# Performance work log

Hardware: AMD Instinct MI355X
Metric: run time of the kernel (lower is better)

## Reference

```python
import jax, jax.numpy as jnp
import numpy as np

L = 32            # num_layers
R = 16            # lora_rank
P = L * 7         # 224 projections
D = 256           # encoder d_model
H = 4             # encoder heads
HD = D // H
FF = 2048         # TransformerEncoderLayer default dim_feedforward
PED = 512         # proj_embed_dim
HID = 4096
KV = 8 * (4096 // 32)   # 1024
INTER = 11008
VOCAB = 50000
NEG = -1e9

# projection index groups within the P=7*L ordering [q,k,v,o,gate,up,down]
IDX_A_HID = jnp.asarray((np.arange(L)[:, None] * 7 + np.array([0, 1, 2, 3, 4, 5])).reshape(-1))  # in_dim=4096
IDX_A_INT = jnp.asarray(np.arange(L) * 7 + 6)                                                    # in_dim=11008
IDX_B_HID = jnp.asarray((np.arange(L)[:, None] * 7 + np.array([0, 3, 6])).reshape(-1))           # out_dim=4096
IDX_B_KV  = jnp.asarray((np.arange(L)[:, None] * 7 + np.array([1, 2])).reshape(-1))              # out_dim=1024
IDX_B_INT = jnp.asarray((np.arange(L)[:, None] * 7 + np.array([4, 5])).reshape(-1))              # out_dim=11008


def _ln(x, g, b, eps=1e-5):
    m = jnp.mean(x, -1, keepdims=True)
    v = jnp.mean((x - m) ** 2, -1, keepdims=True)
    return (x - m) * jax.lax.rsqrt(v + eps) * g + b


def _enc_layer(x, pad, qw, qb, ow, ob, g1, b1, f1w, f1b, f2w, f2b, g2, b2):
    # post-norm TransformerEncoderLayer (torch default), relu FFN, eval mode (no dropout)
    Bsz, S, _ = x.shape
    qkv = x @ qw.T + qb                                  # [B,S,3D]
    q, k, v = jnp.split(qkv, 3, axis=-1)
    hd = lambda t: t.reshape(Bsz, S, H, HD).transpose(0, 2, 1, 3)
    q, k, v = hd(q), hd(k), hd(v)
    s = jnp.einsum('bhqd,bhkd->bhqk', q, k) / jnp.asarray(np.sqrt(HD), x.dtype)
    s = jnp.where(pad[:, None, None, :], NEG, s)
    a = jax.nn.softmax(s, -1)
    o = jnp.einsum('bhqk,bhkd->bhqd', a, v).transpose(0, 2, 1, 3).reshape(Bsz, S, D)
    x = _ln(x + o @ ow.T + ob, g1, b1)
    f = jax.nn.relu(x @ f1w.T + f1b) @ f2w.T + f2b
    return _ln(x + f, g2, b2)


def _forward(condition_ids, attention_mask, embed_table, enc_qkv_w, enc_qkv_b, enc_out_w, enc_out_b,
             enc_ln1_g, enc_ln1_b, enc_ff1_w, enc_ff1_b, enc_ff2_w, enc_ff2_b, enc_ln2_g, enc_ln2_b,
             proj_w, proj_b, a1_w, a1_b, a2_w, a2_b, b1_w, b1_b, b2_w, b2_b, scales):
    Bsz = condition_ids.shape[0]
    x = embed_table[condition_ids]                       # [B,S,256]
    pad = attention_mask == 0                            # key padding mask (~attention_mask)
    for l in range(3):
        x = _enc_layer(x, pad, enc_qkv_w[l], enc_qkv_b[l], enc_out_w[l], enc_out_b[l],
                       enc_ln1_g[l], enc_ln1_b[l], enc_ff1_w[l], enc_ff1_b[l],
                       enc_ff2_w[l], enc_ff2_b[l], enc_ln2_g[l], enc_ln2_b[l])
    am = attention_mask.astype(x.dtype)
    pooled = (x * am[..., None]).sum(1) / jnp.clip(am.sum(1, keepdims=True), 1.0)   # masked mean pool
    pe = (pooled @ proj_w.T + proj_b).reshape(Bsz, P, PED)                          # [B,224,512]

    def dec(w1, b1_, w2, b2_):
        return jax.nn.gelu(pe @ w1.T + b1_, approximate=False) @ w2.T + b2_

    A_base = dec(a1_w, a1_b, a2_w, a2_b).reshape(Bsz, P, R, 64)   # [B,P,r,64]
    B_base = dec(b1_w, b1_b, b2_w, b2_b).reshape(Bsz, P, 64, R)   # [B,P,64,r]
    sa, sb = scales[:, 0], scales[:, 1]

    def tile_A(idx, in_d):
        # all in_dims divisible by 64 => repeat(in_d//64+1)[:, :in_d] == exact tiling
        a = A_base[:, idx] * sa[idx][None, :, None, None]
        return jnp.tile(a, (1, 1, 1, in_d // 64))

    def tile_B(idx, out_d):
        b = B_base[:, idx] * sb[idx][None, :, None, None]
        return jnp.tile(b, (1, 1, out_d // 64, 1))

    return (tile_A(IDX_A_HID, HID), tile_A(IDX_A_INT, INTER),
            tile_B(IDX_B_HID, HID), tile_B(IDX_B_KV, KV), tile_B(IDX_B_INT, INTER))


def setup_inputs() -> dict:
    key = jax.random.key(0)
    ks = iter(jax.random.split(key, 40))
    rn = lambda shape, s=0.02: jax.random.normal(next(ks), shape, jnp.float32) * s
    Bsz, S = 4, 128
    return {
        'condition_ids': jax.random.randint(next(ks), (Bsz, S), 0, VOCAB),
        'attention_mask': jnp.ones((Bsz, S), jnp.int32),
        'embed_table': rn((VOCAB, D)),
        'enc_qkv_w': rn((3, 3 * D, D)), 'enc_qkv_b': rn((3, 3 * D)),
        'enc_out_w': rn((3, D, D)), 'enc_out_b': rn((3, D)),
        'enc_ln1_g': jnp.ones((3, D)), 'enc_ln1_b': jnp.zeros((3, D)),
        'enc_ff1_w': rn((3, FF, D)), 'enc_ff1_b': rn((3, FF)),
        'enc_ff2_w': rn((3, D, FF)), 'enc_ff2_b': rn((3, D)),
        'enc_ln2_g': jnp.ones((3, D)), 'enc_ln2_b': jnp.zeros((3, D)),
        'proj_w': rn((P * PED, D)), 'proj_b': rn((P * PED,)),
        'a1_w': rn((D, PED)), 'a1_b': rn((D,)),
        'a2_w': rn((R * 64, D)), 'a2_b': rn((R * 64,)),
        'b1_w': rn((D, PED)), 'b1_b': rn((D,)),
        'b2_w': rn((R * 64, D)), 'b2_b': rn((R * 64,)),
        'scales': jnp.full((P, 2), 0.01, jnp.float32),
    }


def reference(condition_ids, attention_mask, embed_table, enc_qkv_w, enc_qkv_b, enc_out_w, enc_out_b,
              enc_ln1_g, enc_ln1_b, enc_ff1_w, enc_ff1_b, enc_ff2_w, enc_ff2_b, enc_ln2_g, enc_ln2_b,
              proj_w, proj_b, a1_w, a1_b, a2_w, a2_b, b1_w, b1_b, b2_w, b2_b, scales):
    return _forward(condition_ids, attention_mask, embed_table, enc_qkv_w, enc_qkv_b, enc_out_w, enc_out_b,
                    enc_ln1_g, enc_ln1_b, enc_ff1_w, enc_ff1_b, enc_ff2_w, enc_ff2_b, enc_ln2_g, enc_ln2_b,
                    proj_w, proj_b, a1_w, a1_b, a2_w, a2_b, b1_w, b1_b, b2_w, b2_b, scales)
```

## Files before the change

kernel.cpp:

```cpp
#include <hip/hip_runtime.h>
#include <hip/hip_bf16.h>

typedef unsigned short u16;
typedef unsigned int u32;
typedef __attribute__((ext_vector_type(8))) short short8;
typedef __attribute__((ext_vector_type(4))) float floatx4;

__device__ __forceinline__ u16 f2bf(float f) {
  u32 x = __float_as_uint(f);
  x += 0x7FFFu + ((x >> 16) & 1u);
  return (u16)(x >> 16);
}
__device__ __forceinline__ u32 pk2(float lo, float hi) {
  return (u32)f2bf(lo) | ((u32)f2bf(hi) << 16);
}

__global__ void embed_kernel(const int* __restrict__ ids, const float* __restrict__ emb,
                             float* __restrict__ x) {
  int tok = blockIdx.x, d = threadIdx.x;
  x[tok * 256 + d] = emb[(size_t)ids[tok] * 256 + d];
}

template <int ACT, int SPLIT>
__global__ __launch_bounds__(256) void mfma_gemm_kernel(const float* __restrict__ A,
    const float* __restrict__ W, const float* __restrict__ bias, float* __restrict__ C,
    int M, int N, int K, int KS, int pstride) {
  __shared__ u16 Abf[64 * 32];
  __shared__ u16 Wbf[64 * 32];
  const int t = threadIdx.x;
  const int m0 = blockIdx.x * 64, n0 = blockIdx.y * 64;
  const int kz = blockIdx.z;
  const int srow = t >> 2, skc = (t & 3) * 8;
  const int w = t >> 6, lane = t & 63;
  const int q = lane >> 4, rr = lane & 15;
  floatx4 acc[4];
#pragma unroll
  for (int i = 0; i < 4; ++i) acc[i] = (floatx4){0.f, 0.f, 0.f, 0.f};

  const int kbeg = kz * KS, kend = kbeg + KS;
  for (int k0 = kbeg; k0 < kend; k0 += 32) {
    const float* ga = A + (size_t)(m0 + srow) * K + k0 + skc;
    const float* gw = W + (size_t)(n0 + srow) * K + k0 + skc;
    float4 a0 = *(const float4*)ga;
    float4 a1 = *(const float4*)(ga + 4);
    float4 w0 = *(const float4*)gw;
    float4 w1 = *(const float4*)(gw + 4);
    uint4 pa, pw;
    pa.x = pk2(a0.x, a0.y); pa.y = pk2(a0.z, a0.w);
    pa.z = pk2(a1.x, a1.y); pa.w = pk2(a1.z, a1.w);
    pw.x = pk2(w0.x, w0.y); pw.y = pk2(w0.z, w0.w);
    pw.z = pk2(w1.x, w1.y); pw.w = pk2(w1.z, w1.w);
    __syncthreads();
    *(uint4*)&Abf[srow * 32 + skc] = pa;
    *(uint4*)&Wbf[srow * 32 + skc] = pw;
    __syncthreads();
    short8 af = *(short8*)&Abf[(w * 16 + rr) * 32 + q * 8];
#pragma unroll
    for (int ct = 0; ct < 4; ++ct) {
      short8 bf = *(short8*)&Wbf[(ct * 16 + rr) * 32 + q * 8];
      acc[ct] = __builtin_amdgcn_mfma_f32_16x16x32_bf16(af, bf, acc[ct], 0, 0, 0);
    }
  }

  float* dst = SPLIT ? (C + (size_t)kz * pstride) : C;
#pragma unroll
  for (int ct = 0; ct < 4; ++ct) {
    int col = n0 + ct * 16 + rr;
#pragma unroll
    for (int r = 0; r < 4; ++r) {
      int row = m0 + w * 16 + q * 4 + r;
      float v = acc[ct][r];
      if (!SPLIT) {
        v += bias[col];
        if (ACT == 1) v = fmaxf(v, 0.f);
        if (ACT == 2) v = 0.5f * v * (1.f + erff(v * 0.70710678118654752f));
      }
      dst[(size_t)row * N + col] = v;
    }
  }
}

template <int ACT>
__global__ void red_bias_act_kernel(const float* __restrict__ parts, int nparts, int pstride,
                                    const float* __restrict__ bias, float* __restrict__ dst, int N) {
  int idx = blockIdx.x * 256 + threadIdx.x;
  float v = bias[idx % N];
  for (int p = 0; p < nparts; ++p) v += parts[(size_t)p * pstride + idx];
  if (ACT == 1) v = fmaxf(v, 0.f);
  if (ACT == 2) v = 0.5f * v * (1.f + erff(v * 0.70710678118654752f));
  dst[idx] = v;
}

__global__ __launch_bounds__(256) void attn_kernel(const float* __restrict__ qkv,
    const int* __restrict__ mask, float* __restrict__ o) {
  __shared__ float Klds[8192];
  __shared__ float Vlds[8192];
  const int blk = blockIdx.x;
  const int b = blk >> 7, h = (blk >> 5) & 3, qg = blk & 31;
  const int t = threadIdx.x;
  for (int i = t; i < 8192; i += 256) {
    int s = i >> 6, d = i & 63;
    size_t base = (size_t)(b * 128 + s) * 768 + h * 64 + d;
    Klds[(s << 6) + (d ^ (s & 31))] = qkv[base + 256];
    Vlds[i] = qkv[base + 512];
  }
  __syncthreads();
  const int wave = t >> 6, lane = t & 63;
  const int q = qg * 4 + wave;
  float qv = qkv[(size_t)(b * 128 + q) * 768 + h * 64 + lane];
  const int m0i = mask[b * 128 + lane];
  const int m1i = mask[b * 128 + 64 + lane];
  float s0 = 0.f, s1 = 0.f;
  const int sw = lane & 31;
  for (int d = 0; d < 64; ++d) {
    float qd = __shfl(qv, d);
    s0 += qd * Klds[(lane << 6) + (d ^ sw)];
    s1 += qd * Klds[((lane + 64) << 6) + (d ^ sw)];
  }
  s0 *= 0.125f; s1 *= 0.125f;
  if (m0i == 0) s0 = -1000000000.0f;
  if (m1i == 0) s1 = -1000000000.0f;
  float m = fmaxf(s0, s1);
  for (int off = 32; off; off >>= 1) m = fmaxf(m, __shfl_xor(m, off));
  float p0 = expf(s0 - m), p1 = expf(s1 - m);
  float sum = p0 + p1;
  for (int off = 32; off; off >>= 1) sum += __shfl_xor(sum, off);
  float rs = 1.f / sum;
  float acc = 0.f;
  for (int k = 0; k < 64; ++k) acc += __shfl(p0, k) * Vlds[(k << 6) + lane];
  for (int k = 0; k < 64; ++k) acc += __shfl(p1, k) * Vlds[((k + 64) << 6) + lane];
  o[(size_t)(b * 128 + q) * 256 + h * 64 + lane] = acc * rs;
}

__global__ __launch_bounds__(256) void add_ln_red_kernel(float* __restrict__ x,
    const float* __restrict__ parts, int nparts, int pstride, const float* __restrict__ bias,
    const float* __restrict__ g, const float* __restrict__ b) {
  int tok = blockIdx.x, t = threadIdx.x;
  int idx = tok * 256 + t;
  float r = x[idx] + bias[t];
  for (int p = 0; p < nparts; ++p) r += parts[(size_t)p * pstride + idx];
  float s = r, sq = r * r;
  for (int off = 32; off; off >>= 1) { s += __shfl_xor(s, off); sq += __shfl_xor(sq, off); }
  __shared__ float red[8];
  int wave = t >> 6, lane = t & 63;
  if (lane == 0) { red[wave] = s; red[4 + wave] = sq; }
  __syncthreads();
  float S = red[0] + red[1] + red[2] + red[3];
  float SQ = red[4] + red[5] + red[6] + red[7];
  float mean = S * (1.f / 256.f);
  float var = SQ * (1.f / 256.f) - mean * mean;
  float inv = 1.f / sqrtf(fmaxf(var, 0.f) + 1e-5f);
  x[idx] = (r - mean) * inv * g[t] + b[t];
}

__global__ void pool_kernel(const float* __restrict__ x, const int* __restrict__ mask,
                            float* __restrict__ pooled) {
  int b = blockIdx.x, d = threadIdx.x;
  float s = 0.f, c = 0.f;
  for (int ss = 0; ss < 128; ++ss) {
    float m = (float)mask[b * 128 + ss];
    s += m * x[(size_t)(b * 128 + ss) * 256 + d];
    c += m;
  }
  pooled[b * 256 + d] = s / fmaxf(c, 1.f);
}

__global__ __launch_bounds__(256) void proj_kernel(const float* __restrict__ pooled,
    const float* __restrict__ W, const float* __restrict__ bias, float* __restrict__ pe) {
  __shared__ float pl[1024];
  int t = threadIdx.x;
  for (int i = t; i < 1024; i += 256) pl[i] = pooled[i];
  __syncthreads();
  int wave = t >> 6, lane = t & 63;
  int half = lane >> 5, sl = lane & 31;
  int row = blockIdx.x * 8 + wave * 2 + half;
  float4 w0 = *(const float4*)(W + (size_t)row * 256 + sl * 8);
  float4 w1 = *(const float4*)(W + (size_t)row * 256 + sl * 8 + 4);
  float a0, a1, a2, a3;
#pragma unroll
  for (int bb = 0; bb < 4; ++bb) {
    const float* pp = &pl[bb * 256 + sl * 8];
    float v = w0.x * pp[0] + w0.y * pp[1] + w0.z * pp[2] + w0.w * pp[3]
            + w1.x * pp[4] + w1.y * pp[5] + w1.z * pp[6] + w1.w * pp[7];
    if (bb == 0) a0 = v; else if (bb == 1) a1 = v; else if (bb == 2) a2 = v; else a3 = v;
  }
#pragma unroll
  for (int off = 1; off < 32; off <<= 1) {
    a0 += __shfl_xor(a0, off); a1 += __shfl_xor(a1, off);
    a2 += __shfl_xor(a2, off); a3 += __shfl_xor(a3, off);
  }
  if (sl == 0) {
    float bv = bias[row];
    pe[0 * 114688 + row] = a0 + bv;
    pe[1 * 114688 + row] = a1 + bv;
    pe[2 * 114688 + row] = a2 + bv;
    pe[3 * 114688 + row] = a3 + bv;
  }
}

__global__ __launch_bounds__(256) void tile_a_kernel(const float* __restrict__ Abase,
    const float* __restrict__ scales, float* __restrict__ out, int nI, int ind,
    int pdiv, int pmul, int padd) {
  int row = blockIdx.x;
  int r = row & 15, bi = row >> 4;
  int i = bi % nI, b = bi / nI;
  int p = (i / pdiv) * 7 + (i % pdiv) * pmul + padd;
  float s = scales[2 * p];
  __shared__ float chunk[64];
  int t = threadIdx.x;
  if (t < 64) chunk[t] = Abase[((size_t)(b * 224 + p) * 16 + r) * 64 + t] * s;
  __syncthreads();
  size_t ob = (size_t)row * ind;
  for (int u = t; u * 4 < ind; u += 256) {
    int c0 = u * 4;
    float4 ov = *(const float4*)&chunk[c0 & 63];
    *(float4*)(out + ob + c0) = ov;
  }
}

__global__ __launch_bounds__(256) void tile_b_kernel(const float* __restrict__ Bbase,
    const float* __restrict__ scales, float* __restrict__ out, int nI, int ind, int nchunks,
    int pdiv, int pmul, int padd) {
  int blk = blockIdx.x;
  int cc = blk % nchunks, bi = blk / nchunks;
  int i = bi % nI, b = bi / nI;
  int p = (i / pdiv) * 7 + (i % pdiv) * pmul + padd;
  float s = scales[2 * p + 1];
  __shared__ float chunk[1024];
  int t = threadIdx.x;
  for (int e = t; e < 1024; e += 256) chunk[e] = Bbase[(size_t)(b * 224 + p) * 1024 + e] * s;
  __syncthreads();
  int cchunk16 = (ind / nchunks) * 16;
  size_t ob = (size_t)bi * ind * 16 + (size_t)cc * cchunk16;
  for (int u = t; u * 4 < cchunk16; u += 256) {
    int e0 = u * 4;
    int cabs = (cc * cchunk16 + e0) >> 4;
    int src = ((cabs & 63) << 4) + (e0 & 15);
    float4 ov = *(const float4*)&chunk[src];
    *(float4*)(out + ob + e0) = ov;
  }
}

extern "C" void kernel_launch(void* const* d_in, const int* in_sizes, int n_in,
                              void* d_out, int out_size, void* d_ws, size_t ws_size,
                              hipStream_t stream) {
  const int* ids     = (const int*)d_in[0];
  const int* mask    = (const int*)d_in[1];
  const float* emb   = (const float*)d_in[2];
  const float* qkv_w = (const float*)d_in[3];
  const float* qkv_b = (const float*)d_in[4];
  const float* out_w = (const float*)d_in[5];
  const float* out_b = (const float*)d_in[6];
  const float* ln1_g = (const float*)d_in[7];
  const float* ln1_b = (const float*)d_in[8];
  const float* ff1_w = (const float*)d_in[9];
  const float* ff1_b = (const float*)d_in[10];
  const float* ff2_w = (const float*)d_in[11];
  const float* ff2_b = (const float*)d_in[12];
  const float* ln2_g = (const float*)d_in[13];
  const float* ln2_b = (const float*)d_in[14];
  const float* proj_w = (const float*)d_in[15];
  const float* proj_b = (const float*)d_in[16];
  const float* a1_w = (const float*)d_in[17];
  const float* a1_b = (const float*)d_in[18];
  const float* a2_w = (const float*)d_in[19];
  const float* a2_b = (const float*)d_in[20];
  const float* b1_w = (const float*)d_in[21];
  const float* b1_b = (const float*)d_in[22];
  const float* b2_w = (const float*)d_in[23];
  const float* b2_b = (const float*)d_in[24];
  const float* scales = (const float*)d_in[25];

  float* w = (float*)d_ws;
  float* x      = w + 0;
  float* qkv    = w + 262144;
  float* attn_o = w + 655360;
  float* ff     = w + 786432;
  float* pooled = w + 1835008;
  float* pe     = w + 1836032;
  float* hA     = w + 2294784;
  float* hB     = w + 2524160;
  float* Abase  = w + 2753536;
  float* Bbase  = w + 3671040;
  float* parts  = w + 4588544;

  float* out = (float*)d_out;

  embed_kernel<<<512, 256, 0, stream>>>(ids, emb, x);
  for (int l = 0; l < 3; ++l) {
    mfma_gemm_kernel<0, 0><<<dim3(8, 12), 256, 0, stream>>>(
        x, qkv_w + l * 768 * 256, qkv_b + l * 768, qkv, 512, 768, 256, 256, 0);
    attn_kernel<<<512, 256, 0, stream>>>(qkv, mask, attn_o);
    mfma_gemm_kernel<0, 1><<<dim3(8, 4, 4), 256, 0, stream>>>(
        attn_o, out_w + l * 256 * 256, nullptr, parts, 512, 256, 256, 64, 131072);
    add_ln_red_kernel<<<512, 256, 0, stream>>>(x, parts, 4, 131072, out_b + l * 256,
                                               ln1_g + l * 256, ln1_b + l * 256);
    mfma_gemm_kernel<1, 0><<<dim3(8, 32), 256, 0, stream>>>(
        x, ff1_w + l * 2048 * 256, ff1_b + l * 2048, ff, 512, 2048, 256, 256, 0);
    mfma_gemm_kernel<0, 1><<<dim3(8, 4, 8), 256, 0, stream>>>(
        ff, ff2_w + l * 256 * 2048, nullptr, parts, 512, 256, 2048, 256, 131072);
    add_ln_red_kernel<<<512, 256, 0, stream>>>(x, parts, 8, 131072, ff2_b + l * 256,
                                               ln2_g + l * 256, ln2_b + l * 256);
  }
  pool_kernel<<<4, 256, 0, stream>>>(x, mask, pooled);
  proj_kernel<<<14336, 256, 0, stream>>>(pooled, proj_w, proj_b, pe);

  mfma_gemm_kernel<0, 1><<<dim3(14, 4, 4), 256, 0, stream>>>(
      pe, a1_w, nullptr, parts, 896, 256, 512, 128, 229376);
  red_bias_act_kernel<2><<<896, 256, 0, stream>>>(parts, 4, 229376, a1_b, hA, 256);
  mfma_gemm_kernel<0, 0><<<dim3(14, 16), 256, 0, stream>>>(
      hA, a2_w, a2_b, Abase, 896, 1024, 256, 256, 0);

  mfma_gemm_kernel<0, 1><<<dim3(14, 4, 4), 256, 0, stream>>>(
      pe, b1_w, nullptr, parts, 896, 256, 512, 128, 229376);
  red_bias_act_kernel<2><<<896, 256, 0, stream>>>(parts, 4, 229376, b1_b, hB, 256);
  mfma_gemm_kernel<0, 0><<<dim3(14, 16), 256, 0, stream>>>(
      hB, b2_w, b2_b, Bbase, 896, 1024, 256, 256, 0);

  tile_a_kernel<<<12288, 256, 0, stream>>>(Abase, scales, out, 192, 4096, 6, 1, 0);
  tile_a_kernel<<<2048, 256, 0, stream>>>(Abase, scales, out + 50331648ull, 32, 11008, 1, 0, 6);
  tile_b_kernel<<<3072, 256, 0, stream>>>(Bbase, scales, out + 72876032ull, 96, 4096, 8, 3, 3, 0);
  tile_b_kernel<<<512, 256, 0, stream>>>(Bbase, scales, out + 98041856ull, 64, 1024, 2, 2, 1, 1);
  tile_b_kernel<<<2048, 256, 0, stream>>>(Bbase, scales, out + 102236160ull, 64, 11008, 8, 2, 1, 4);
}
```

Before: 974.3 us.

## Fuse encoder layers and decoder GEMMs with output tiling using bf16 intermediates

Rewrites most of the pipeline. Weights are pre-converted to bf16 once per call. Each encoder layer becomes fused kernels: out-proj, residual, LayerNorm and FF1 in one, and FF2, LayerNorm and next-layer QKV in another, with bf16 activations between them. The LoRA decoder GEMMs are fused with the scale-and-tile broadcast writes, which removes the intermediate Abase/Bbase buffers and the split-K partial reductions. The cost is that the fused encoder kernels run only 16 blocks, which leaves most of the GPU idle. There is also extra bf16 rounding of intermediates.

```diff
diff --git a/kernel.cpp b/kernel.cpp
--- a/kernel.cpp
+++ b/kernel.cpp
@@ -11,88 +11,113 @@
   x += 0x7FFFu + ((x >> 16) & 1u);
   return (u16)(x >> 16);
 }
-__device__ __forceinline__ u32 pk2(float lo, float hi) {
-  return (u32)f2bf(lo) | ((u32)f2bf(hi) << 16);
-}
-
-__global__ void embed_kernel(const int* __restrict__ ids, const float* __restrict__ emb,
-                             float* __restrict__ x) {
-  int tok = blockIdx.x, d = threadIdx.x;
-  x[tok * 256 + d] = emb[(size_t)ids[tok] * 256 + d];
-}
-
-template <int ACT, int SPLIT>
-__global__ __launch_bounds__(256) void mfma_gemm_kernel(const float* __restrict__ A,
-    const float* __restrict__ W, const float* __restrict__ bias, float* __restrict__ C,
-    int M, int N, int K, int KS, int pstride) {
-  __shared__ u16 Abf[64 * 32];
-  __shared__ u16 Wbf[64 * 32];
-  const int t = threadIdx.x;
-  const int m0 = blockIdx.x * 64, n0 = blockIdx.y * 64;
-  const int kz = blockIdx.z;
-  const int srow = t >> 2, skc = (t & 3) * 8;
-  const int w = t >> 6, lane = t & 63;
-  const int q = lane >> 4, rr = lane & 15;
-  floatx4 acc[4];
-#pragma unroll
-  for (int i = 0; i < 4; ++i) acc[i] = (floatx4){0.f, 0.f, 0.f, 0.f};
-
-  const int kbeg = kz * KS, kend = kbeg + KS;
-  for (int k0 = kbeg; k0 < kend; k0 += 32) {
-    const float* ga = A + (size_t)(m0 + srow) * K + k0 + skc;
-    const float* gw = W + (size_t)(n0 + srow) * K + k0 + skc;
-    float4 a0 = *(const float4*)ga;
-    float4 a1 = *(const float4*)(ga + 4);
-    float4 w0 = *(const float4*)gw;
-    float4 w1 = *(const float4*)(gw + 4);
-    uint4 pa, pw;
-    pa.x = pk2(a0.x, a0.y); pa.y = pk2(a0.z, a0.w);
-    pa.z = pk2(a1.x, a1.y); pa.w = pk2(a1.z, a1.w);
-    pw.x = pk2(w0.x, w0.y); pw.y = pk2(w0.z, w0.w);
-    pw.z = pk2(w1.x, w1.y); pw.w = pk2(w1.z, w1.w);
-    __syncthreads();
-    *(uint4*)&Abf[srow * 32 + skc] = pa;
-    *(uint4*)&Wbf[srow * 32 + skc] = pw;
-    __syncthreads();
-    short8 af = *(short8*)&Abf[(w * 16 + rr) * 32 + q * 8];
-#pragma unroll
-    for (int ct = 0; ct < 4; ++ct) {
-      short8 bf = *(short8*)&Wbf[(ct * 16 + rr) * 32 + q * 8];
-      acc[ct] = __builtin_amdgcn_mfma_f32_16x16x32_bf16(af, bf, acc[ct], 0, 0, 0);
-    }
-  }
-
-  float* dst = SPLIT ? (C + (size_t)kz * pstride) : C;
-#pragma unroll
-  for (int ct = 0; ct < 4; ++ct) {
-    int col = n0 + ct * 16 + rr;
-#pragma unroll
-    for (int r = 0; r < 4; ++r) {
-      int row = m0 + w * 16 + q * 4 + r;
-      float v = acc[ct][r];
-      if (!SPLIT) {
-        v += bias[col];
-        if (ACT == 1) v = fmaxf(v, 0.f);
-        if (ACT == 2) v = 0.5f * v * (1.f + erff(v * 0.70710678118654752f));
+__device__ __forceinline__ float bf2f(u16 u) { return __uint_as_float(((u32)u) << 16); }
+
+__device__ __forceinline__ void mfma8(floatx4& acc, short8 a, short8 b) {
+  acc = __builtin_amdgcn_mfma_f32_16x16x32_bf16(a, b, acc, 0, 0, 0);
+}
+
+#define ZACC24(A)                    \
+  do {                               \
+    for (int _i = 0; _i < 2; ++_i)   \
+      for (int _j = 0; _j < 4; ++_j) \
+        A[_i][_j] = (floatx4){0.f, 0.f, 0.f, 0.f}; \
+  } while (0)
+
+__device__ __forceinline__ void gemm_tile_lA(floatx4 acc[2][4], const u16* Abf, int lda,
+                                             const u16* W, int ldw, int n0, int K, int lane) {
+  const int rr = lane & 15, q = lane >> 4;
+  for (int k0 = 0; k0 < K; k0 += 32) {
+    short8 a0 = *(const short8*)(Abf + rr * lda + k0 + q * 8);
+    short8 a1 = *(const short8*)(Abf + (16 + rr) * lda + k0 + q * 8);
+#pragma unroll
+    for (int nt = 0; nt < 4; ++nt) {
+      short8 b = *(const short8*)(W + (size_t)(n0 + nt * 16 + rr) * ldw + k0 + q * 8);
+      mfma8(acc[0][nt], a0, b);
+      mfma8(acc[1][nt], a1, b);
+    }
+  }
+}
+
+__device__ __forceinline__ void gemm_tile_gA(floatx4 acc[2][4], const u16* Ag, int lda, int m0,
+                                             const u16* W, int ldw, int n0, int K, int lane) {
+  const int rr = lane & 15, q = lane >> 4;
+  for (int k0 = 0; k0 < K; k0 += 32) {
+    short8 a0 = *(const short8*)(Ag + (size_t)(m0 + rr) * lda + k0 + q * 8);
+    short8 a1 = *(const short8*)(Ag + (size_t)(m0 + 16 + rr) * lda + k0 + q * 8);
+#pragma unroll
+    for (int nt = 0; nt < 4; ++nt) {
+      short8 b = *(const short8*)(W + (size_t)(n0 + nt * 16 + rr) * ldw + k0 + q * 8);
+      mfma8(acc[0][nt], a0, b);
+      mfma8(acc[1][nt], a1, b);
+    }
+  }
+}
+
+__device__ __forceinline__ void store_cd_bf16(floatx4 acc[2][4], u16* dst, int ld, int m0,
+                                              int n0, const float* bias, int relu, int lane) {
+  const int rr = lane & 15, q = lane >> 4;
+#pragma unroll
+  for (int mt = 0; mt < 2; ++mt)
+#pragma unroll
+    for (int nt = 0; nt < 4; ++nt) {
+      int col = n0 + nt * 16 + rr;
+      float bv = bias[col];
+#pragma unroll
+      for (int r = 0; r < 4; ++r) {
+        int row = m0 + mt * 16 + q * 4 + r;
+        float v = acc[mt][nt][r] + bv;
+        if (relu) v = fmaxf(v, 0.f);
+        dst[(size_t)row * ld + col] = f2bf(v);
       }
-      dst[(size_t)row * N + col] = v;
-    }
-  }
-}
-
-template <int ACT>
-__global__ void red_bias_act_kernel(const float* __restrict__ parts, int nparts, int pstride,
-                                    const float* __restrict__ bias, float* __restrict__ dst, int N) {
-  int idx = blockIdx.x * 256 + threadIdx.x;
-  float v = bias[idx % N];
-  for (int p = 0; p < nparts; ++p) v += parts[(size_t)p * pstride + idx];
-  if (ACT == 1) v = fmaxf(v, 0.f);
-  if (ACT == 2) v = 0.5f * v * (1.f + erff(v * 0.70710678118654752f));
-  dst[idx] = v;
-}
-
-__global__ __launch_bounds__(256) void attn_kernel(const float* __restrict__ qkv,
-    const int* __restrict__ mask, float* __restrict__ o) {
+    }
+}
+
+struct WConvArgs {
+  const float* src[8];
+  u16* dst[8];
+  int cnt[8];
+};
+__global__ __launch_bounds__(256) void wconv_kernel(WConvArgs a) {
+  int tid = blockIdx.x * 256 + threadIdx.x;
+  int stride = gridDim.x * 256;
+  for (int s = 0; s < 8; ++s) {
+    const float* src = a.src[s];
+    u16* dst = a.dst[s];
+    int n4 = a.cnt[s] >> 2;
+    for (int i = tid; i < n4; i += stride) {
+      float4 v = ((const float4*)src)[i];
+      ushort4 o;
+      o.x = f2bf(v.x); o.y = f2bf(v.y); o.z = f2bf(v.z); o.w = f2bf(v.w);
+      ((ushort4*)dst)[i] = o;
+    }
+  }
+}
+
+__global__ __launch_bounds__(256) void embed_qkv_kernel(const int* __restrict__ ids,
+    const float* __restrict__ emb, float* __restrict__ x, const u16* __restrict__ qkvw,
+    const float* __restrict__ qkvb, u16* __restrict__ qkvbf) {
+  __shared__ u16 Albs[32 * 256];
+  const int rb = blockIdx.x, t = threadIdx.x, w = t >> 6, lane = t & 63;
+  const int m0 = rb * 32;
+  for (int r = 0; r < 32; ++r) {
+    int row = m0 + r;
+    float v = emb[(size_t)ids[row] * 256 + t];
+    x[(size_t)row * 256 + t] = v;
+    Albs[r * 256 + t] = f2bf(v);
+  }
+  __syncthreads();
+  for (int g = 0; g < 3; ++g) {
+    floatx4 acc[2][4];
+    ZACC24(acc);
+    int n0 = w * 192 + g * 64;
+    gemm_tile_lA(acc, Albs, 256, qkvw, 256, n0, 256, lane);
+    store_cd_bf16(acc, qkvbf, 768, m0, n0, qkvb, 0, lane);
+  }
+}
+
+__global__ __launch_bounds__(256) void attn_kernel(const u16* __restrict__ qkv,
+    const int* __restrict__ mask, u16* __restrict__ o) {
   __shared__ float Klds[8192];
   __shared__ float Vlds[8192];
   const int blk = blockIdx.x;
@@ -101,13 +126,13 @@
   for (int i = t; i < 8192; i += 256) {
     int s = i >> 6, d = i & 63;
     size_t base = (size_t)(b * 128 + s) * 768 + h * 64 + d;
-    Klds[(s << 6) + (d ^ (s & 31))] = qkv[base + 256];
-    Vlds[i] = qkv[base + 512];
+    Klds[(s << 6) + (d ^ (s & 31))] = bf2f(qkv[base + 256]);
+    Vlds[i] = bf2f(qkv[base + 512]);
   }
   __syncthreads();
   const int wave = t >> 6, lane = t & 63;
   const int q = qg * 4 + wave;
-  float qv = qkv[(size_t)(b * 128 + q) * 768 + h * 64 + lane];
+  float qv = bf2f(qkv[(size_t)(b * 128 + q) * 768 + h * 64 + lane]);
   const int m0i = mask[b * 128 + lane];
   const int m1i = mask[b * 128 + 64 + lane];
   float s0 = 0.f, s1 = 0.f;
@@ -129,28 +154,124 @@
   float acc = 0.f;
   for (int k = 0; k < 64; ++k) acc += __shfl(p0, k) * Vlds[(k << 6) + lane];
   for (int k = 0; k < 64; ++k) acc += __shfl(p1, k) * Vlds[((k + 64) << 6) + lane];
-  o[(size_t)(b * 128 + q) * 256 + h * 64 + lane] = acc * rs;
-}
-
-__global__ __launch_bounds__(256) void add_ln_red_kernel(float* __restrict__ x,
-    const float* __restrict__ parts, int nparts, int pstride, const float* __restrict__ bias,
-    const float* __restrict__ g, const float* __restrict__ b) {
-  int tok = blockIdx.x, t = threadIdx.x;
-  int idx = tok * 256 + t;
-  float r = x[idx] + bias[t];
-  for (int p = 0; p < nparts; ++p) r += parts[(size_t)p * pstride + idx];
-  float s = r, sq = r * r;
-  for (int off = 32; off; off >>= 1) { s += __shfl_xor(s, off); sq += __shfl_xor(sq, off); }
-  __shared__ float red[8];
-  int wave = t >> 6, lane = t & 63;
-  if (lane == 0) { red[wave] = s; red[4 + wave] = sq; }
-  __syncthreads();
-  float S = red[0] + red[1] + red[2] + red[3];
-  float SQ = red[4] + red[5] + red[6] + red[7];
-  float mean = S * (1.f / 256.f);
-  float var = SQ * (1.f / 256.f) - mean * mean;
-  float inv = 1.f / sqrtf(fmaxf(var, 0.f) + 1e-5f);
-  x[idx] = (r - mean) * inv * g[t] + b[t];
+  o[(size_t)(b * 128 + q) * 256 + h * 64 + lane] = f2bf(acc * rs);
+}
+
+__global__ __launch_bounds__(256) void post1_kernel(float* __restrict__ x,
+    const u16* __restrict__ obf, const u16* __restrict__ outw, const float* __restrict__ outb,
+    const float* __restrict__ g1, const float* __restrict__ b1, const u16* __restrict__ ff1w,
+    const float* __restrict__ ff1b, u16* __restrict__ ffbf) {
+  __shared__ u16 Albs[32 * 256];
+  __shared__ float S[32 * 264];
+  const int rb = blockIdx.x, t = threadIdx.x, w = t >> 6, lane = t & 63;
+  const int m0 = rb * 32;
+  {
+    const uint4* src = (const uint4*)(obf + (size_t)m0 * 256);
+    uint4* dst = (uint4*)Albs;
+    for (int i = t; i < 1024; i += 256) dst[i] = src[i];
+  }
+  __syncthreads();
+  floatx4 acc[2][4];
+  ZACC24(acc);
+  gemm_tile_lA(acc, Albs, 256, outw, 256, w * 64, 256, lane);
+  {
+    const int rr = lane & 15, q = lane >> 4;
+#pragma unroll
+    for (int mt = 0; mt < 2; ++mt)
+#pragma unroll
+      for (int nt = 0; nt < 4; ++nt) {
+        int col = w * 64 + nt * 16 + rr;
+        float bv = outb[col];
+#pragma unroll
+        for (int r = 0; r < 4; ++r) {
+          int row = mt * 16 + q * 4 + r;
+          S[row * 264 + col] = acc[mt][nt][r] + bv + x[(size_t)(m0 + row) * 256 + col];
+        }
+      }
+  }
+  __syncthreads();
+  {
+    int j = t >> 3, s8 = t & 7;
+    float sm = 0.f, sq = 0.f;
+    for (int c = s8 * 32; c < s8 * 32 + 32; ++c) {
+      float v = S[j * 264 + c];
+      sm += v; sq += v * v;
+    }
+    for (int off = 1; off < 8; off <<= 1) { sm += __shfl_xor(sm, off); sq += __shfl_xor(sq, off); }
+    float mean = sm * (1.f / 256.f);
+    float var = sq * (1.f / 256.f) - mean * mean;
+    float inv = 1.f / sqrtf(fmaxf(var, 0.f) + 1e-5f);
+    for (int c = s8 * 32; c < s8 * 32 + 32; ++c) {
+      float v = (S[j * 264 + c] - mean) * inv * g1[c] + b1[c];
+      x[(size_t)(m0 + j) * 256 + c] = v;
+      Albs[j * 256 + c] = f2bf(v);
+    }
+  }
+  __syncthreads();
+  for (int gb = 0; gb < 8; ++gb) {
+    floatx4 a2[2][4];
+    ZACC24(a2);
+    int n0 = w * 512 + gb * 64;
+    gemm_tile_lA(a2, Albs, 256, ff1w, 256, n0, 256, lane);
+    store_cd_bf16(a2, ffbf, 2048, m0, n0, ff1b, 1, lane);
+  }
+}
+
+template <int LAST>
+__global__ __launch_bounds__(256) void post2_kernel(const u16* __restrict__ ffbf,
+    const u16* __restrict__ ff2w, const float* __restrict__ ff2b, const float* __restrict__ g2,
+    const float* __restrict__ b2, float* __restrict__ x, const u16* __restrict__ qkvw,
+    const float* __restrict__ qkvb, u16* __restrict__ qkvbf) {
+  __shared__ u16 Albs[32 * 256];
+  __shared__ float S[32 * 264];
+  const int rb = blockIdx.x, t = threadIdx.x, w = t >> 6, lane = t & 63;
+  const int m0 = rb * 32;
+  floatx4 acc[2][4];
+  ZACC24(acc);
+  gemm_tile_gA(acc, ffbf, 2048, m0, ff2w, 2048, w * 64, 2048, lane);
+  {
+    const int rr = lane & 15, q = lane >> 4;
+#pragma unroll
+    for (int mt = 0; mt < 2; ++mt)
+#pragma unroll
+      for (int nt = 0; nt < 4; ++nt) {
+        int col = w * 64 + nt * 16 + rr;
+        float bv = ff2b[col];
+#pragma unroll
+        for (int r = 0; r < 4; ++r) {
+          int row = mt * 16 + q * 4 + r;
+          S[row * 264 + col] = acc[mt][nt][r] + bv + x[(size_t)(m0 + row) * 256 + col];
+        }
+      }
+  }
+  __syncthreads();
+  {
+    int j = t >> 3, s8 = t & 7;
+    float sm = 0.f, sq = 0.f;
+    for (int c = s8 * 32; c < s8 * 32 + 32; ++c) {
+      float v = S[j * 264 + c];
+      sm += v; sq += v * v;
+    }
+    for (int off = 1; off < 8; off <<= 1) { sm += __shfl_xor(sm, off); sq += __shfl_xor(sq, off); }
+    float mean = sm * (1.f / 256.f);
+    float var = sq * (1.f / 256.f) - mean * mean;
+    float inv = 1.f / sqrtf(fmaxf(var, 0.f) + 1e-5f);
+    for (int c = s8 * 32; c < s8 * 32 + 32; ++c) {
+      float v = (S[j * 264 + c] - mean) * inv * g2[c] + b2[c];
+      x[(size_t)(m0 + j) * 256 + c] = v;
+      Albs[j * 256 + c] = f2bf(v);
+    }
+  }
+  __syncthreads();
+  if (!LAST) {
+    for (int g = 0; g < 3; ++g) {
+      floatx4 a2[2][4];
+      ZACC24(a2);
+      int n0 = w * 192 + g * 64;
+      gemm_tile_lA(a2, Albs, 256, qkvw, 256, n0, 256, lane);
+      store_cd_bf16(a2, qkvbf, 768, m0, n0, qkvb, 0, lane);
+    }
+  }
 }
 
 __global__ void pool_kernel(const float* __restrict__ x, const int* __restrict__ mask,
@@ -166,7 +287,7 @@
 }
 
 __global__ __launch_bounds__(256) void proj_kernel(const float* __restrict__ pooled,
-    const float* __restrict__ W, const float* __restrict__ bias, float* __restrict__ pe) {
+    const float* __restrict__ W, const float* __restrict__ bias, u16* __restrict__ pebf) {
   __shared__ float pl[1024];
   int t = threadIdx.x;
   for (int i = t; i < 1024; i += 256) pl[i] = pooled[i];
@@ -191,53 +312,133 @@
   }
   if (sl == 0) {
     float bv = bias[row];
-    pe[0 * 114688 + row] = a0 + bv;
-    pe[1 * 114688 + row] = a1 + bv;
-    pe[2 * 114688 + row] = a2 + bv;
-    pe[3 * 114688 + row] = a3 + bv;
-  }
-}
-
-__global__ __launch_bounds__(256) void tile_a_kernel(const float* __restrict__ Abase,
-    const float* __restrict__ scales, float* __restrict__ out, int nI, int ind,
-    int pdiv, int pmul, int padd) {
-  int row = blockIdx.x;
-  int r = row & 15, bi = row >> 4;
-  int i = bi % nI, b = bi / nI;
-  int p = (i / pdiv) * 7 + (i % pdiv) * pmul + padd;
-  float s = scales[2 * p];
-  __shared__ float chunk[64];
-  int t = threadIdx.x;
-  if (t < 64) chunk[t] = Abase[((size_t)(b * 224 + p) * 16 + r) * 64 + t] * s;
-  __syncthreads();
-  size_t ob = (size_t)row * ind;
-  for (int u = t; u * 4 < ind; u += 256) {
-    int c0 = u * 4;
-    float4 ov = *(const float4*)&chunk[c0 & 63];
-    *(float4*)(out + ob + c0) = ov;
-  }
-}
-
-__global__ __launch_bounds__(256) void tile_b_kernel(const float* __restrict__ Bbase,
-    const float* __restrict__ scales, float* __restrict__ out, int nI, int ind, int nchunks,
-    int pdiv, int pmul, int padd) {
-  int blk = blockIdx.x;
-  int cc = blk % nchunks, bi = blk / nchunks;
-  int i = bi % nI, b = bi / nI;
-  int p = (i / pdiv) * 7 + (i % pdiv) * pmul + padd;
-  float s = scales[2 * p + 1];
-  __shared__ float chunk[1024];
-  int t = threadIdx.x;
-  for (int e = t; e < 1024; e += 256) chunk[e] = Bbase[(size_t)(b * 224 + p) * 1024 + e] * s;
-  __syncthreads();
-  int cchunk16 = (ind / nchunks) * 16;
-  size_t ob = (size_t)bi * ind * 16 + (size_t)cc * cchunk16;
-  for (int u = t; u * 4 < cchunk16; u += 256) {
-    int e0 = u * 4;
-    int cabs = (cc * cchunk16 + e0) >> 4;
-    int src = ((cabs & 63) << 4) + (e0 & 15);
-    float4 ov = *(const float4*)&chunk[src];
-    *(float4*)(out + ob + e0) = ov;
+    pebf[0 * 114688 + row] = f2bf(a0 + bv);
+    pebf[1 * 114688 + row] = f2bf(a1 + bv);
+    pebf[2 * 114688 + row] = f2bf(a2 + bv);
+    pebf[3 * 114688 + row] = f2bf(a3 + bv);
+  }
+}
+
+__global__ __launch_bounds__(256) void dec1_kernel(const u16* __restrict__ pebf,
+    const u16* __restrict__ a1w, const u16* __restrict__ b1w, const float* __restrict__ a1b,
+    const float* __restrict__ b1b, u16* __restrict__ hA, u16* __restrict__ hB) {
+  const int rb = blockIdx.x, zi = blockIdx.y;
+  const u16* W = zi ? b1w : a1w;
+  const float* bias = zi ? b1b : a1b;
+  u16* dst = zi ? hB : hA;
+  const int t = threadIdx.x, w = t >> 6, lane = t & 63;
+  const int m0 = rb * 32;
+  floatx4 acc[2][4];
+  ZACC24(acc);
+  gemm_tile_gA(acc, pebf, 512, m0, W, 512, w * 64, 512, lane);
+  const int rr = lane & 15, q = lane >> 4;
+#pragma unroll
+  for (int mt = 0; mt < 2; ++mt)
+#pragma unroll
+    for (int nt = 0; nt < 4; ++nt) {
+      int col = w * 64 + nt * 16 + rr;
+      float bv = bias[col];
+#pragma unroll
+      for (int r = 0; r < 4; ++r) {
+        int row = m0 + mt * 16 + q * 4 + r;
+        float v = acc[mt][nt][r] + bv;
+        v = 0.5f * v * (1.f + erff(v * 0.70710678118654752f));
+        dst[(size_t)row * 256 + col] = f2bf(v);
+      }
+    }
+}
+
+__global__ __launch_bounds__(256) void dec2a_kernel(const u16* __restrict__ hA,
+    const u16* __restrict__ a2w, const float* __restrict__ a2b, const float* __restrict__ scales,
+    float* __restrict__ out0, float* __restrict__ out1) {
+  __shared__ float tile[32][68];
+  const int rb = blockIdx.x, j = blockIdx.y, z = blockIdx.z;
+  const int t = threadIdx.x, w = t >> 6, lane = t & 63;
+  const int m0 = rb * 32;
+  const int mt = w >> 1, ntb = (w & 1) * 2;
+  const int rr = lane & 15, q = lane >> 4;
+  floatx4 acc[2];
+  acc[0] = (floatx4){0.f, 0.f, 0.f, 0.f};
+  acc[1] = (floatx4){0.f, 0.f, 0.f, 0.f};
+  for (int k0 = 0; k0 < 256; k0 += 32) {
+    short8 a = *(const short8*)(hA + (size_t)(m0 + mt * 16 + rr) * 256 + k0 + q * 8);
+#pragma unroll
+    for (int u = 0; u < 2; ++u) {
+      short8 b = *(const short8*)(a2w + (size_t)(j * 64 + (ntb + u) * 16 + rr) * 256 + k0 + q * 8);
+      mfma8(acc[u], a, b);
+    }
+  }
+#pragma unroll
+  for (int u = 0; u < 2; ++u) {
+    int lc = (ntb + u) * 16 + rr;
+    float bv = a2b[j * 64 + lc];
+#pragma unroll
+    for (int r = 0; r < 4; ++r) tile[mt * 16 + q * 4 + r][lc] = acc[u][r] + bv;
+  }
+  __syncthreads();
+  const int c = (t * 4) & 63;
+  for (int r = 0; r < 32; ++r) {
+    int bp = m0 + r, b = bp / 224, p = bp % 224, l7 = p / 7, k7 = p % 7;
+    float s = scales[2 * p];
+    float4 v;
+    v.x = tile[r][c] * s; v.y = tile[r][c + 1] * s;
+    v.z = tile[r][c + 2] * s; v.w = tile[r][c + 3] * s;
+    if (k7 < 6) {
+      size_t base = ((size_t)((b * 192 + l7 * 6 + k7) * 16 + j)) * 4096 + z * 1024;
+      *(float4*)(out0 + base + t * 4) = v;
+    } else {
+      size_t base = ((size_t)((b * 32 + l7) * 16 + j)) * 11008 + z * 2752;
+      for (int i = t * 4; i < 2752; i += 1024) *(float4*)(out1 + base + i) = v;
+    }
+  }
+}
+
+__global__ __launch_bounds__(256) void dec2b_kernel(const u16* __restrict__ hB,
+    const u16* __restrict__ b2w, const float* __restrict__ b2b, const float* __restrict__ scales,
+    float* __restrict__ out2, float* __restrict__ out3, float* __restrict__ out4) {
+  __shared__ float tile[32][68];
+  const int rb = blockIdx.x, j = blockIdx.y, z = blockIdx.z;
+  const int t = threadIdx.x, w = t >> 6, lane = t & 63;
+  const int m0 = rb * 32;
+  const int mt = w >> 1, ntb = (w & 1) * 2;
+  const int rr = lane & 15, q = lane >> 4;
+  floatx4 acc[2];
+  acc[0] = (floatx4){0.f, 0.f, 0.f, 0.f};
+  acc[1] = (floatx4){0.f, 0.f, 0.f, 0.f};
+  for (int k0 = 0; k0 < 256; k0 += 32) {
+    short8 a = *(const short8*)(hB + (size_t)(m0 + mt * 16 + rr) * 256 + k0 + q * 8);
+#pragma unroll
+    for (int u = 0; u < 2; ++u) {
+      short8 b = *(const short8*)(b2w + (size_t)(j * 64 + (ntb + u) * 16 + rr) * 256 + k0 + q * 8);
+      mfma8(acc[u], a, b);
+    }
+  }
+#pragma unroll
+  for (int u = 0; u < 2; ++u) {
+    int lc = (ntb + u) * 16 + rr;
+    float bv = b2b[j * 64 + lc];
+#pragma unroll
+    for (int r = 0; r < 4; ++r) tile[mt * 16 + q * 4 + r][lc] = acc[u][r] + bv;
+  }
+  __syncthreads();
+  const int r16 = t & 15, c_l = (t >> 4) & 3, wv = t >> 6;
+  for (int r = 0; r < 32; ++r) {
+    int bp = m0 + r, b = bp / 224, p = bp % 224, l7 = p / 7, k7 = p % 7;
+    float s = scales[2 * p + 1];
+    float v = tile[r][c_l * 16 + r16] * s;
+    if (k7 == 0 || k7 == 3 || k7 == 6) {
+      size_t rowbase = (size_t)(b * 96 + l7 * 3 + k7 / 3) * 65536;
+      for (int rep = z * 16 + wv; rep < z * 16 + 16; rep += 4)
+        out2[rowbase + (size_t)(rep * 64 + j * 4 + c_l) * 16 + r16] = v;
+    } else if (k7 <= 2) {
+      size_t rowbase = (size_t)(b * 64 + l7 * 2 + (k7 - 1)) * 16384;
+      int rep = z * 4 + wv;
+      out3[rowbase + (size_t)(rep * 64 + j * 4 + c_l) * 16 + r16] = v;
+    } else {
+      size_t rowbase = (size_t)(b * 64 + l7 * 2 + (k7 - 4)) * 176128;
+      for (int rep = z * 43 + wv; rep < z * 43 + 43; rep += 4)
+        out4[rowbase + (size_t)(rep * 64 + j * 4 + c_l) * 16 + r16] = v;
+    }
   }
 }
 
@@ -271,55 +472,61 @@
   const float* b2_b = (const float*)d_in[24];
   const float* scales = (const float*)d_in[25];
 
-  float* w = (float*)d_ws;
-  float* x      = w + 0;
-  float* qkv    = w + 262144;
-  float* attn_o = w + 655360;
-  float* ff     = w + 786432;
-  float* pooled = w + 1835008;
-  float* pe     = w + 1836032;
-  float* hA     = w + 2294784;
-  float* hB     = w + 2524160;
-  float* Abase  = w + 2753536;
-  float* Bbase  = w + 3671040;
-  float* parts  = w + 4588544;
+  u16* wb = (u16*)d_ws;
+  u16* qkvw_b = wb + 0;
+  u16* outw_b = wb + 589824;
+  u16* ff1w_b = wb + 786432;
+  u16* ff2w_b = wb + 2359296;
+  u16* a1w_b  = wb + 3932160;
+  u16* a2w_b  = wb + 4063232;
+  u16* b1w_b  = wb + 4325376;
+  u16* b2w_b  = wb + 4456448;
+  u16* qkvbf  = wb + 4718592;
+  u16* obf    = wb + 5111808;
+  u16* ffbf   = wb + 5242880;
+  u16* pebf   = wb + 6291456;
+  u16* hAbf   = wb + 6750208;
+  u16* hBbf   = wb + 6979584;
+  float* xbuf   = (float*)(wb + 7208960);
+  float* pooled = xbuf + 131072;
 
   float* out = (float*)d_out;
-
-  embed_kernel<<<512, 256, 0, stream>>>(ids, emb, x);
+  float* out0 = out;
+  float* out1 = out + 50331648ull;
+  float* out2 = out + 72876032ull;
+  float* out3 = out + 98041856ull;
+  float* out4 = out + 102236160ull;
+
+  WConvArgs wa;
+  wa.src[0] = qkv_w; wa.dst[0] = qkvw_b; wa.cnt[0] = 589824;
+  wa.src[1] = out_w; wa.dst[1] = outw_b; wa.cnt[1] = 196608;
+  wa.src[2] = ff1_w; wa.dst[2] = ff1w_b; wa.cnt[2] = 1572864;
+  wa.src[3] = ff2_w; wa.dst[3] = ff2w_b; wa.cnt[3] = 1572864;
+  wa.src[4] = a1_w;  wa.dst[4] = a1w_b;  wa.cnt[4] = 131072;
+  wa.src[5] = a2_w;  wa.dst[5] = a2w_b;  wa.cnt[5] = 262144;
+  wa.src[6] = b1_w;  wa.dst[6] = b1w_b;  wa.cnt[6] = 131072;
+  wa.src[7] = b2_w;  wa.dst[7] = b2w_b;  wa.cnt[7] = 262144;
+  wconv_kernel<<<1024, 256, 0, stream>>>(wa);
+
+  embed_qkv_kernel<<<16, 256, 0, stream>>>(ids, emb, xbuf, qkvw_b, qkv_b, qkvbf);
   for (int l = 0; l < 3; ++l) {
-    mfma_gemm_kernel<0, 0><<<dim3(8, 12), 256, 0, stream>>>(
-        x, qkv_w + l * 768 * 256, qkv_b + l * 768, qkv, 512, 768, 256, 256, 0);
-    attn_kernel<<<512, 256, 0, stream>>>(qkv, mask, attn_o);
-    mfma_gemm_kernel<0, 1><<<dim3(8, 4, 4), 256, 0, stream>>>(
-        attn_o, out_w + l * 256 * 256, nullptr, parts, 512, 256, 256, 64, 131072);
-    add_ln_red_kernel<<<512, 256, 0, stream>>>(x, parts, 4, 131072, out_b + l * 256,
-                                               ln1_g + l * 256, ln1_b + l * 256);
-    mfma_gemm_kernel<1, 0><<<dim3(8, 32), 256, 0, stream>>>(
-        x, ff1_w + l * 2048 * 256, ff1_b + l * 2048, ff, 512, 2048, 256, 256, 0);
-    mfma_gemm_kernel<0, 1><<<dim3(8, 4, 8), 256, 0, stream>>>(
-        ff, ff2_w + l * 256 * 2048, nullptr, parts, 512, 256, 2048, 256, 131072);
-    add_ln_red_kernel<<<512, 256, 0, stream>>>(x, parts, 8, 131072, ff2_b + l * 256,
-                                               ln2_g + l * 256, ln2_b + l * 256);
-  }
-  pool_kernel<<<4, 256, 0, stream>>>(x, mask, pooled);
-  proj_kernel<<<14336, 256, 0, stream>>>(pooled, proj_w, proj_b, pe);
-
-  mfma_gemm_kernel<0, 1><<<dim3(14, 4, 4), 256, 0, stream>>>(
-      pe, a1_w, nullptr, parts, 896, 256, 512, 128, 229376);
-  red_bias_act_kernel<2><<<896, 256, 0, stream>>>(parts, 4, 229376, a1_b, hA, 256);
-  mfma_gemm_kernel<0, 0><<<dim3(14, 16), 256, 0, stream>>>(
-      hA, a2_w, a2_b, Abase, 896, 1024, 256, 256, 0);
-
-  mfma_gemm_kernel<0, 1><<<dim3(14, 4, 4), 256, 0, stream>>>(
-      pe, b1_w, nullptr, parts, 896, 256, 512, 128, 229376);
-  red_bias_act_kernel<2><<<896, 256, 0, stream>>>(parts, 4, 229376, b1_b, hB, 256);
-  mfma_gemm_kernel<0, 0><<<dim3(14, 16), 256, 0, stream>>>(
-      hB, b2_w, b2_b, Bbase, 896, 1024, 256, 256, 0);
-
-  tile_a_kernel<<<12288, 256, 0, stream>>>(Abase, scales, out, 192, 4096, 6, 1, 0);
-  tile_a_kernel<<<2048, 256, 0, stream>>>(Abase, scales, out + 50331648ull, 32, 11008, 1, 0, 6);
-  tile_b_kernel<<<3072, 256, 0, stream>>>(Bbase, scales, out + 72876032ull, 96, 4096, 8, 3, 3, 0);
-  tile_b_kernel<<<512, 256, 0, stream>>>(Bbase, scales, out + 98041856ull, 64, 1024, 2, 2, 1, 1);
-  tile_b_kernel<<<2048, 256, 0, stream>>>(Bbase, scales, out + 102236160ull, 64, 11008, 8, 2, 1, 4);
-}
+    attn_kernel<<<512, 256, 0, stream>>>(qkvbf, mask, obf);
+    post1_kernel<<<16, 256, 0, stream>>>(xbuf, obf, outw_b + l * 65536, out_b + l * 256,
+                                         ln1_g + l * 256, ln1_b + l * 256,
+                                         ff1w_b + l * 524288, ff1_b + l * 2048, ffbf);
+    if (l < 2)
+      post2_kernel<0><<<16, 256, 0, stream>>>(ffbf, ff2w_b + l * 524288, ff2_b + l * 256,
+                                              ln2_g + l * 256, ln2_b + l * 256, xbuf,
+                                              qkvw_b + (l + 1) * 196608, qkv_b + (l + 1) * 768,
+                                              qkvbf);
+    else
+      post2_kernel<1><<<16, 256, 0, stream>>>(ffbf, ff2w_b + l * 524288, ff2_b + l * 256,
+                                              ln2_g + l * 256, ln2_b + l * 256, xbuf,
+                                              qkvw_b, qkv_b, qkvbf);
+  }
+  pool_kernel<<<4, 256, 0, stream>>>(xbuf, mask, pooled);
+  proj_kernel<<<14336, 256, 0, stream>>>(pooled, proj_w, proj_b, pebf);
+  dec1_kernel<<<dim3(28, 2), 256, 0, stream>>>(pebf, a1w_b, b1w_b, a1_b, b1_b, hAbf, hBbf);
+  dec2a_kernel<<<dim3(28, 16, 4), 256, 0, stream>>>(hAbf, a2w_b, a2_b, scales, out0, out1);
+  dec2b_kernel<<<dim3(28, 16, 4), 256, 0, stream>>>(hBbf, b2w_b, b2_b, scales, out2, out3, out4);
+}
```

Result: slower. 1.291 ms (+32.5%).
